# Kernel optimization log

Measured on AMD Instinct MI355X. Metric: run time of the kernel, lower is better.

## Reference

```python
import jax, jax.numpy as jnp
import numpy as np

# dims: n=batch, T=n_shifts, dX=16, dU=8, H=256 hidden, L=128 ldim, K=64 n_aux (L=2K)

def setup_inputs() -> dict:
    key = jax.random.key(0)
    ks = jax.random.split(key, 16)
    n, T, dX, dU, H, L, K = 64, 64, 16, 8, 256, 128, 64
    def lin(k, fan_in, shape):
        return (jax.random.uniform(k, shape, jnp.float32) * 2.0 - 1.0) / np.sqrt(fan_in)
    xs = jax.random.normal(ks[0], (n, T, dX), jnp.float32)
    us = jax.random.normal(ks[1], (n, T - 1, dU), jnp.float32)
    theta = jax.random.uniform(ks[2], (K,), jnp.float32) * (2.0 * np.pi)
    inp = {
        'xs': xs, 'us': us,
        # stacked x-aux encoders (K copies): BN affine, 3 linear layers (last no bias), output scale
        'x_gamma': jnp.ones((K, dX)), 'x_beta': jnp.zeros((K, dX)),
        'xW1': lin(ks[3], dX, (K, dX, H)), 'xb1': jnp.zeros((K, H)),
        'xW2': lin(ks[4], H, (K, H, H)), 'xb2': jnp.zeros((K, H)),
        'xW3': lin(ks[5], H, (K, H, L)), 'x_scale': jnp.ones((K, L)),
        # stacked u-aux encoders (K copies)
        'u_gamma': jnp.ones((K, dU)), 'u_beta': jnp.zeros((K, dU)),
        'uW1': lin(ks[6], dU, (K, dU, H)), 'ub1': jnp.zeros((K, H)),
        'uW2': lin(ks[7], H, (K, H, H)), 'ub2': jnp.zeros((K, H)),
        'uW3': lin(ks[8], H, (K, H, L)), 'u_scale': jnp.ones((K, L)),
        # Jordan-block complex eigenvalues (|lam| ~ 0.95)
        'reL': 0.95 * jnp.cos(theta), 'imL': 0.95 * jnp.sin(theta),
        # decoder C: Linear(ldim, dim, bias=False) -> weight [dX, L]
        'C_W': lin(ks[9], L, (dX, L)),
    }
    return inp


def _encoder(x, gamma, beta, W1, b1, W2, b2, W3, scale):
    # x: [M, D]; stacked params over K nets. BN stats (training mode) are per-feature over M,
    # identical across nets since the same x feeds every net.
    mu = x.mean(0)
    var = ((x - mu) ** 2).mean(0)
    xn = (x - mu) * jax.lax.rsqrt(var + 1e-5)          # [M, D]
    h = xn[None] * gamma[:, None, :] + beta[:, None, :]  # [K, M, D]
    h = jax.nn.leaky_relu(jnp.einsum('kmd,kdh->kmh', h, W1) + b1[:, None, :])
    h = jax.nn.leaky_relu(jnp.einsum('kmd,kdh->kmh', h, W2) + b2[:, None, :])
    h = jnp.einsum('kmd,kdh->kmh', h, W3)               # last layer: no bias
    return h * scale[:, None, :]                        # [K, M, L]


def reference(xs, us, x_gamma, x_beta, xW1, xb1, xW2, xb2, xW3, x_scale,
              u_gamma, u_beta, uW1, ub1, uW2, ub2, uW3, u_scale, reL, imL, C_W):
    n, T, dX = xs.shape
    K = reL.shape[0]
    L = 2 * K
    Tm1 = T - 1
    # phi1s: [n, T, K(net), K(pair), 2]
    phi = _encoder(xs.reshape(n * T, dX), x_gamma, x_beta, xW1, xb1, xW2, xb2, xW3, x_scale)
    phi1s = jnp.moveaxis(phi, 0, 1).reshape(n, T, K, K, 2)
    # ures = psi(u) - psi(0): [n, T-1, K, K, 2]
    uflat = us.reshape(n * Tm1, -1)
    psi_u = _encoder(uflat, u_gamma, u_beta, uW1, ub1, uW2, ub2, uW3, u_scale)
    psi_0 = _encoder(jnp.zeros_like(uflat), u_gamma, u_beta, uW1, ub1, uW2, ub2, uW3, u_scale)
    ures = jnp.moveaxis(psi_u - psi_0, 0, 1).reshape(n, Tm1, K, K, 2)
    # block-diagonal Koopman: per net j a 2x2 rotation-scale [[re, im], [-im, re]]
    R = jnp.stack([jnp.stack([reL, imL], -1), jnp.stack([-imL, reL], -1)], -2)  # [K, 2, 2]

    def step(p, u_t):
        p = jnp.einsum('bjkc,jcd->bjkd', p + u_t, R)
        return p, p

    _, preds = jax.lax.scan(step, phi1s[:, 0], jnp.moveaxis(ures, 0, 1))
    preds = jnp.moveaxis(preds, 0, 1)  # [n, T-1, K, K, 2]

    def phi2y(p):
        # sum over net axis (-3), flatten pair dims -> [.., L], decode with C
        return p.sum(-3).reshape(*p.shape[:-3], L) @ C_W.T

    y = phi2y(phi1s[:, 1:])
    y_pred = phi2y(preds)
    return y, y_pred
```

## Files before the change

kernel.cpp:

```cpp
#include <hip/hip_runtime.h>

typedef __bf16 bf16_t;
typedef __bf16 bf16x8 __attribute__((ext_vector_type(8)));
typedef __bf16 bf16x4 __attribute__((ext_vector_type(4)));
typedef float  f32x4  __attribute__((ext_vector_type(4)));

#define PHI_JS  (4096 * 128 + 64)
#define PSIU_JS (4032 * 128 + 64)

__global__ __launch_bounds__(256) void prep_all_kernel(
    const float* __restrict__ xW1, const float* __restrict__ xb1,
    const float* __restrict__ xg,  const float* __restrict__ xbeta,
    const float* __restrict__ uW1, const float* __restrict__ ub1,
    const float* __restrict__ ug,  const float* __restrict__ ubeta,
    const float* __restrict__ xW2, const float* __restrict__ uW2,
    const float* __restrict__ xW3, const float* __restrict__ uW3,
    const float* __restrict__ x_scale, const float* __restrict__ u_scale,
    const float* __restrict__ xs, const float* __restrict__ us,
    bf16_t* __restrict__ xW1t, float* __restrict__ xb1p,
    bf16_t* __restrict__ uW1t, float* __restrict__ ub1p,
    bf16_t* __restrict__ xW2t, bf16_t* __restrict__ uW2t,
    bf16_t* __restrict__ xW3t, bf16_t* __restrict__ uW3t,
    float* __restrict__ part, float* __restrict__ zout)
{
    const int t = blockIdx.x, tid = threadIdx.x;
    __shared__ float tile[32][33];
    __shared__ float h1[256], h2[256];

    if (t < 12288) {
        const float* in; bf16_t* outp; const float* scale = nullptr;
        int j, r0, c0, C;
        if (t < 8192) {
            C = 256;
            j = (t & 4095) >> 6;
            const int tl = t & 63; r0 = (tl >> 3) * 32; c0 = (tl & 7) * 32;
            if (t < 4096) { in = xW2; outp = xW2t; }
            else          { in = uW2; outp = uW2t; }
        } else {
            C = 128;
            const int l = t - 8192;
            j = (l & 2047) >> 5;
            const int tl = l & 31; r0 = (tl >> 2) * 32; c0 = (tl & 3) * 32;
            if (l < 2048) { in = xW3; outp = xW3t; scale = x_scale + j * 128; }
            else          { in = uW3; outp = uW3t; scale = u_scale + j * 128; }
        }
        const int R = 256;
        in   += (size_t)j * R * C;
        bf16_t* op = outp + (size_t)j * R * C;
        const int tx = tid & 31, ty = tid >> 5;
        #pragma unroll
        for (int i = 0; i < 4; i++)
            tile[ty + i * 8][tx] = in[(size_t)(r0 + ty + i * 8) * C + c0 + tx];
        __syncthreads();
        #pragma unroll
        for (int i = 0; i < 4; i++) {
            int c = c0 + ty + i * 8;
            float sc = scale ? scale[c] : 1.f;
            op[(size_t)c * R + r0 + tx] = (bf16_t)(tile[tx][ty + i * 8] * sc);
        }
    } else if (t < 12416) {
        const int bid = t - 12288, j = bid & 63, h = tid;
        const float *W1, *b1, *gamma, *beta; bf16_t* W1t; float* b1p; int D;
        if (bid < 64) { W1 = xW1; b1 = xb1; gamma = xg; beta = xbeta; W1t = xW1t; b1p = xb1p; D = 16; }
        else          { W1 = uW1; b1 = ub1; gamma = ug; beta = ubeta; W1t = uW1t; b1p = ub1p; D = 8; }
        float bacc = b1[j * 256 + h];
        bf16_t* orow = W1t + (size_t)(j * 256 + h) * 32;
        for (int d = 0; d < 32; d++) orow[d] = (bf16_t)0.f;
        for (int d = 0; d < D; d++) {
            float w = W1[((size_t)j * D + d) * 256 + h];
            orow[d] = (bf16_t)(gamma[j * D + d] * w);
            bacc += beta[j * D + d] * w;
        }
        b1p[j * 256 + h] = bacc;
    } else if (t < 12512) {
        const int bid = t - 12416;
        const bool isx = bid < 64;
        const float* x = isx ? xs : us;
        const int D   = isx ? 16 : 8;
        const int lb  = isx ? bid : bid - 64;
        const int per = isx ? 1024 : 1008;
        const int start = lb * per;
        float a = 0.f, b = 0.f;
        for (int idx = start + tid; idx < start + per; idx += 256) {
            float v = x[idx];
            a += v; b += v * v;
        }
        float* s1 = h1; float* s2 = h2;
        s1[tid] = a; s2[tid] = b;
        __syncthreads();
        if (tid < D) {
            float sa = 0.f, sb = 0.f;
            for (int k = tid; k < 256; k += D) { sa += s1[k]; sb += s2[k]; }
            part[bid * 32 + tid]      = sa;
            part[bid * 32 + 16 + tid] = sb;
        }
    } else {
        const int g = (t - 12512) * 256 + tid;
        for (int i = g; i < 2 * 64 * 63 * 16; i += 64 * 256)
            zout[i] = 0.f;
    }
}

__global__ __launch_bounds__(512, 4) void fused_mlp_kernel(
    const float* __restrict__ xs, const float* __restrict__ us,
    const float* __restrict__ part,
    const bf16_t* __restrict__ xW1t, const float* __restrict__ xb1p,
    const bf16_t* __restrict__ xW2t, const float* __restrict__ xb2,
    const bf16_t* __restrict__ xW3t,
    const bf16_t* __restrict__ uW1t, const float* __restrict__ ub1p,
    const bf16_t* __restrict__ uW2t, const float* __restrict__ ub2,
    const bf16_t* __restrict__ uW3t,
    const float* __restrict__ uW1r, const float* __restrict__ ub1r,
    const float* __restrict__ ubetar, const float* __restrict__ uW2r,
    const float* __restrict__ uW3r, const float* __restrict__ u_scaler,
    float* __restrict__ psi0_out,
    bf16_t* __restrict__ phi, bf16_t* __restrict__ psiu)
{
    const int bid  = blockIdx.x;
    const int tid  = threadIdx.x;

    __shared__ __align__(16) bf16_t hs[128 * 256];
    __shared__ float stats_s[32];

    if (bid >= 4096) {
        const int j = bid - 4096;
        float* fb  = (float*)hs;
        float* h1  = fb;
        float* h2  = fb + 256;
        float* tmp = fb + 512;
        const int h = tid & 255, half = tid >> 8;
        if (half == 0) {
            float bacc = ub1r[j * 256 + h];
            #pragma unroll
            for (int d = 0; d < 8; d++)
                bacc += ubetar[j * 8 + d] * uW1r[((size_t)j * 8 + d) * 256 + h];
            h1[h] = fmaxf(bacc, 0.01f * bacc);
        }
        __syncthreads();
        {
            float acc = (half == 0) ? ub2[j * 256 + h] : 0.f;
            const float* w2 = uW2r + (size_t)j * 65536 + (size_t)half * 128 * 256 + h;
            #pragma unroll 16
            for (int d = 0; d < 128; d++) acc += h1[half * 128 + d] * w2[(size_t)d * 256];
            tmp[tid] = acc;
        }
        __syncthreads();
        if (half == 0) {
            float v = tmp[h] + tmp[h + 256];
            h2[h] = fmaxf(v, 0.01f * v);
        }
        __syncthreads();
        {
            const int h3 = tid & 127, qd = tid >> 7;
            float acc = 0.f;
            const float* w3 = uW3r + (size_t)j * 32768 + (size_t)qd * 64 * 128 + h3;
            #pragma unroll 16
            for (int d = 0; d < 64; d++) acc += h2[qd * 64 + d] * w3[(size_t)d * 128];
            tmp[tid] = acc;
        }
        __syncthreads();
        if (tid < 128)
            psi0_out[j * 128 + tid] =
                (tmp[tid] + tmp[tid + 128] + tmp[tid + 256] + tmp[tid + 384])
                * u_scaler[j * 128 + tid];
        return;
    }

    const int xcd  = bid & 7;
    const int slot = bid >> 3;
    const int band = slot >> 6;
    const int t64  = slot & 63;
    const int j    = xcd * 8 + band;
    const bool is_x = t64 < 32;
    const int tile  = is_x ? t64 : (t64 - 32);

    const float*  In  = is_x ? xs   : us;
    const int     D   = is_x ? 16   : 8;
    const bf16_t* W1t = is_x ? xW1t : uW1t;
    const float*  b1p = is_x ? xb1p : ub1p;
    const bf16_t* W2t = is_x ? xW2t : uW2t;
    const float*  b2  = is_x ? xb2  : ub2;
    const bf16_t* W3t = is_x ? xW3t : uW3t;
    bf16_t* outp      = is_x ? phi  : psiu;
    const int M       = is_x ? 4096 : 4032;
    const size_t JS   = is_x ? (size_t)PHI_JS : (size_t)PSIU_JS;

    const int row0 = tile * 128;
    const int wave = tid >> 6;
    const int lane = tid & 63;
    const int quad = lane >> 4;
    const int l16  = lane & 15;
    const int lo2  = l16 & 3, hi2 = l16 >> 2;

    if (tid < 16) {
        if (is_x) {
            float sa = 0.f, sb = 0.f;
            #pragma unroll 8
            for (int b = 0; b < 64; b++) { sa += part[b * 32 + tid]; sb += part[b * 32 + 16 + tid]; }
            float mu = sa / 4096.f, var = sb / 4096.f - mu * mu;
            stats_s[tid] = mu; stats_s[16 + tid] = rsqrtf(var + 1e-5f);
        } else if (tid < 8) {
            float sa = 0.f, sb = 0.f;
            #pragma unroll 8
            for (int b = 64; b < 96; b++) { sa += part[b * 32 + tid]; sb += part[b * 32 + 16 + tid]; }
            float mu = sa / 4032.f, var = sb / 4032.f - mu * mu;
            stats_s[tid] = mu; stats_s[16 + tid] = rsqrtf(var + 1e-5f);
        }
    }
    __syncthreads();

    const f32x4 vzero = {0.f, 0.f, 0.f, 0.f};

    char* const hsB = (char*)hs;
    const char* const abase = hsB + l16 * 512 + ((quad ^ lo2) << 4);
    const int  wlow0 = (quad >> 1) ^ lo2;
    char* const wbase = hsB + l16 * 512 + ((wave ^ hi2) << 6) + ((quad & 1) << 3);

    {
        bf16x8 wfr[2];
        #pragma unroll
        for (int nbi = 0; nbi < 2; nbi++)
            wfr[nbi] = *reinterpret_cast<const bf16x8*>(
                W1t + (size_t)(j * 256 + wave * 32 + nbi * 16 + l16) * 32 + quad * 8);

        f32x4 acc[8][2];
        #pragma unroll
        for (int a = 0; a < 8; a++) { acc[a][0] = vzero; acc[a][1] = vzero; }

        const int c0 = quad * 8;
        #pragma unroll
        for (int mb = 0; mb < 8; mb++) {
            bf16x8 a;
            if (c0 < D) {
                int row = row0 + mb * 16 + l16;
                if (row > M - 1) row = M - 1;
                const float* xp = In + (size_t)row * D + c0;
                f32x4 v0 = *reinterpret_cast<const f32x4*>(xp);
                f32x4 v1 = *reinterpret_cast<const f32x4*>(xp + 4);
                #pragma unroll
                for (int e = 0; e < 4; e++) a[e]     = (bf16_t)((v0[e] - stats_s[c0 + e])     * stats_s[16 + c0 + e]);
                #pragma unroll
                for (int e = 0; e < 4; e++) a[4 + e] = (bf16_t)((v1[e] - stats_s[c0 + 4 + e]) * stats_s[16 + c0 + 4 + e]);
            } else {
                #pragma unroll
                for (int e = 0; e < 8; e++) a[e] = (bf16_t)0.f;
            }
            #pragma unroll
            for (int nbi = 0; nbi < 2; nbi++)
                acc[mb][nbi] = __builtin_amdgcn_mfma_f32_16x16x32_bf16(
                    wfr[nbi], a, acc[mb][nbi], 0, 0, 0);
        }

        #pragma unroll
        for (int nbi = 0; nbi < 2; nbi++) {
            const f32x4 bias = *reinterpret_cast<const f32x4*>(
                b1p + j * 256 + wave * 32 + nbi * 16 + quad * 4);
            char* wp = wbase + ((wlow0 ^ (nbi << 1)) << 4);
            #pragma unroll
            for (int mb = 0; mb < 8; mb++) {
                bf16x4 pk;
                #pragma unroll
                for (int r = 0; r < 4; r++) {
                    float v = acc[mb][nbi][r] + bias[r];
                    v = fmaxf(v, 0.01f * v);
                    pk[r] = (bf16_t)v;
                }
                *reinterpret_cast<bf16x4*>(wp + mb * 8192) = pk;
            }
        }
    }
    __syncthreads();

    {
        f32x4 acc[8][2];
        #pragma unroll
        for (int a = 0; a < 8; a++) { acc[a][0] = vzero; acc[a][1] = vzero; }

        const bf16_t* w2base = W2t + ((size_t)j * 256 + wave * 32 + l16) * 256 + quad * 8;

        bf16x8 wr[3][2];
        #pragma unroll
        for (int d = 0; d < 3; d++)
            #pragma unroll
            for (int nbi = 0; nbi < 2; nbi++)
                wr[d][nbi] = *reinterpret_cast<const bf16x8*>(w2base + nbi * 4096 + d * 32);

        #pragma unroll
        for (int kk = 0; kk < 8; kk++) {
            const int c = kk % 3;
            const char* ap = abase + ((kk ^ hi2) << 6);
            bf16x8 av0[4];
            #pragma unroll
            for (int mb = 0; mb < 4; mb++)
                av0[mb] = *reinterpret_cast<const bf16x8*>(ap + mb * 8192);
            #pragma unroll
            for (int nbi = 0; nbi < 2; nbi++)
                #pragma unroll
                for (int mb = 0; mb < 4; mb++)
                    acc[mb][nbi] = __builtin_amdgcn_mfma_f32_16x16x32_bf16(
                        wr[c][nbi], av0[mb], acc[mb][nbi], 0, 0, 0);
            bf16x8 av1[4];
            #pragma unroll
            for (int mb = 0; mb < 4; mb++)
                av1[mb] = *reinterpret_cast<const bf16x8*>(ap + (mb + 4) * 8192);
            #pragma unroll
            for (int nbi = 0; nbi < 2; nbi++)
                #pragma unroll
                for (int mb = 4; mb < 8; mb++)
                    acc[mb][nbi] = __builtin_amdgcn_mfma_f32_16x16x32_bf16(
                        wr[c][nbi], av1[mb - 4], acc[mb][nbi], 0, 0, 0);
            if (kk < 5) {
                #pragma unroll
                for (int nbi = 0; nbi < 2; nbi++)
                    wr[c][nbi] = *reinterpret_cast<const bf16x8*>(
                        w2base + nbi * 4096 + (kk + 3) * 32);
            }
        }
        __syncthreads();
        #pragma unroll
        for (int nbi = 0; nbi < 2; nbi++) {
            const f32x4 bias = *reinterpret_cast<const f32x4*>(
                b2 + j * 256 + wave * 32 + nbi * 16 + quad * 4);
            char* wp = wbase + ((wlow0 ^ (nbi << 1)) << 4);
            #pragma unroll
            for (int mb = 0; mb < 8; mb++) {
                bf16x4 pk;
                #pragma unroll
                for (int r = 0; r < 4; r++) {
                    float v = acc[mb][nbi][r] + bias[r];
                    v = fmaxf(v, 0.01f * v);
                    pk[r] = (bf16_t)v;
                }
                *reinterpret_cast<bf16x4*>(wp + mb * 8192) = pk;
            }
        }
    }
    __syncthreads();

    {
        f32x4 acc[8];
        #pragma unroll
        for (int a = 0; a < 8; a++) acc[a] = vzero;

        const bf16_t* w3base = W3t + ((size_t)j * 128 + wave * 16 + l16) * 256 + quad * 8;

        bf16x8 wr[3];
        #pragma unroll
        for (int d = 0; d < 3; d++)
            wr[d] = *reinterpret_cast<const bf16x8*>(w3base + d * 32);

        #pragma unroll
        for (int kk = 0; kk < 8; kk++) {
            const int c = kk % 3;
            const char* ap = abase + ((kk ^ hi2) << 6);
            bf16x8 av0[4];
            #pragma unroll
            for (int mb = 0; mb < 4; mb++)
                av0[mb] = *reinterpret_cast<const bf16x8*>(ap + mb * 8192);
            #pragma unroll
            for (int mb = 0; mb < 4; mb++)
                acc[mb] = __builtin_amdgcn_mfma_f32_16x16x32_bf16(
                    wr[c], av0[mb], acc[mb], 0, 0, 0);
            bf16x8 av1[4];
            #pragma unroll
            for (int mb = 0; mb < 4; mb++)
                av1[mb] = *reinterpret_cast<const bf16x8*>(ap + (mb + 4) * 8192);
            #pragma unroll
            for (int mb = 4; mb < 8; mb++)
                acc[mb] = __builtin_amdgcn_mfma_f32_16x16x32_bf16(
                    wr[c], av1[mb - 4], acc[mb], 0, 0, 0);
            if (kk < 5)
                wr[c] = *reinterpret_cast<const bf16x8*>(w3base + (kk + 3) * 32);
        }
        __syncthreads();
        {
            const int sp3 = (wave * 2 + (quad >> 1)) ^ l16;
            char* w3p = hsB + l16 * 256 + sp3 * 16 + ((quad & 1) << 3);
            #pragma unroll
            for (int mb = 0; mb < 8; mb++) {
                bf16x4 pk;
                #pragma unroll
                for (int r = 0; r < 4; r++) pk[r] = (bf16_t)acc[mb][r];
                *reinterpret_cast<bf16x4*>(w3p + mb * 4096) = pk;
            }
        }
    }
    __syncthreads();
    #pragma unroll
    for (int p = 0; p < 4; p++) {
        const int rr = p * 32 + (tid >> 4);
        const int s  = tid & 15;
        if (row0 + rr < M) {
            bf16x8 v = *reinterpret_cast<const bf16x8*>(hs + rr * 128 + (s ^ (rr & 15)) * 8);
            *reinterpret_cast<bf16x8*>(outp + (size_t)j * JS + (size_t)(row0 + rr) * 128 + s * 8) = v;
        }
    }
}

__global__ __launch_bounds__(256) void scan_kernel(
    const bf16_t* __restrict__ phi, const bf16_t* __restrict__ psiu,
    const float* __restrict__ psi0, const float* __restrict__ reL,
    const float* __restrict__ imL, const float* __restrict__ C_W,
    float* __restrict__ y, float* __restrict__ ypred) {
    const int b = blockIdx.x >> 3, jg = blockIdx.x & 7;
    const int tid = threadIdx.x;
    const int wave = tid >> 6, lane = tid & 63;
    __shared__ float redP[2][4][128];
    __shared__ float redY[2][4][128];
    __shared__ float SP[128], SY[128];
    __shared__ float Cs[2048];
    #pragma unroll
    for (int i = 0; i < 8; i++) Cs[tid + i * 256] = C_W[tid + i * 256];

    const int j0 = jg * 8 + wave * 2;
    float sx0, sy0, sx1, sy1;
    float p0x0, p0y0, p0x1, p0y1, lre0, lim0, lre1, lim1;
    {
        unsigned v0 = *reinterpret_cast<const unsigned*>(
            phi + (size_t)j0 * PHI_JS + (size_t)(b * 64) * 128 + lane * 2);
        unsigned v1 = *reinterpret_cast<const unsigned*>(
            phi + (size_t)(j0 + 1) * PHI_JS + (size_t)(b * 64) * 128 + lane * 2);
        sx0 = __uint_as_float(v0 << 16); sy0 = __uint_as_float(v0 & 0xFFFF0000u);
        sx1 = __uint_as_float(v1 << 16); sy1 = __uint_as_float(v1 & 0xFFFF0000u);
        float2 p0 = *reinterpret_cast<const float2*>(psi0 + j0 * 128 + lane * 2);
        float2 p1 = *reinterpret_cast<const float2*>(psi0 + (j0 + 1) * 128 + lane * 2);
        p0x0 = p0.x; p0y0 = p0.y; p0x1 = p1.x; p0y1 = p1.y;
        lre0 = reL[j0]; lim0 = imL[j0]; lre1 = reL[j0 + 1]; lim1 = imL[j0 + 1];
    }
    const bf16_t* up0 = psiu + (size_t)j0 * PSIU_JS + (size_t)(b * 63) * 128 + lane * 2;
    const bf16_t* up1 = psiu + (size_t)(j0 + 1) * PSIU_JS + (size_t)(b * 63) * 128 + lane * 2;
    const bf16_t* pp0 = phi + (size_t)j0 * PHI_JS + (size_t)(b * 64 + 1) * 128 + lane * 2;
    const bf16_t* pp1 = phi + (size_t)(j0 + 1) * PHI_JS + (size_t)(b * 64 + 1) * 128 + lane * 2;
    unsigned cur0 = *reinterpret_cast<const unsigned*>(up0);
    unsigned cur1 = *reinterpret_cast<const unsigned*>(up1);
    unsigned curp0 = *reinterpret_cast<const unsigned*>(pp0);
    unsigned curp1 = *reinterpret_cast<const unsigned*>(pp1);

    const int oo = (tid & 127) >> 3, qq = tid & 7;

    for (int t = 0; t < 63; t++) {
        unsigned nx0 = 0, nx1 = 0, np0 = 0, np1 = 0;
        if (t < 62) {
            nx0 = *reinterpret_cast<const unsigned*>(up0 + (t + 1) * 128);
            nx1 = *reinterpret_cast<const unsigned*>(up1 + (t + 1) * 128);
            np0 = *reinterpret_cast<const unsigned*>(pp0 + (t + 1) * 128);
            np1 = *reinterpret_cast<const unsigned*>(pp1 + (t + 1) * 128);
        }
        float px = sx0 + (__uint_as_float(cur0 << 16) - p0x0);
        float py = sy0 + (__uint_as_float(cur0 & 0xFFFF0000u) - p0y0);
        sx0 = px * lre0 - py * lim0;
        sy0 = px * lim0 + py * lre0;
        px = sx1 + (__uint_as_float(cur1 << 16) - p0x1);
        py = sy1 + (__uint_as_float(cur1 & 0xFFFF0000u) - p0y1);
        sx1 = px * lre1 - py * lim1;
        sy1 = px * lim1 + py * lre1;
        float yx = __uint_as_float(curp0 << 16) + __uint_as_float(curp1 << 16);
        float yy = __uint_as_float(curp0 & 0xFFFF0000u) + __uint_as_float(curp1 & 0xFFFF0000u);
        const int db = t & 1;
        redP[db][wave][lane * 2]     = sx0 + sx1;
        redP[db][wave][lane * 2 + 1] = sy0 + sy1;
        redY[db][wave][lane * 2]     = yx;
        redY[db][wave][lane * 2 + 1] = yy;
        __syncthreads();
        if (tid < 128)
            SP[tid] = redP[db][0][tid] + redP[db][1][tid]
                    + redP[db][2][tid] + redP[db][3][tid];
        else {
            const int tl = tid - 128;
            SY[tl] = redY[db][0][tl] + redY[db][1][tl]
                   + redY[db][2][tl] + redY[db][3][tl];
        }
        __syncthreads();
        {
            const float* S = (tid < 128) ? SP : SY;
            float acc = 0.f;
            #pragma unroll
            for (int i = 0; i < 16; i++)
                acc += S[qq * 16 + i] * Cs[oo * 128 + qq * 16 + i];
            acc += __shfl_xor(acc, 4, 8);
            acc += __shfl_xor(acc, 2, 8);
            acc += __shfl_xor(acc, 1, 8);
            if (qq == 0) {
                float* dst = (tid < 128) ? (ypred + (b * 63 + t) * 16 + oo)
                                         : (y     + (b * 63 + t) * 16 + oo);
                atomicAdd(dst, acc);
            }
        }
        cur0 = nx0; cur1 = nx1; curp0 = np0; curp1 = np1;
    }
}

extern "C" void kernel_launch(void* const* d_in, const int* in_sizes, int n_in,
                              void* d_out, int out_size, void* d_ws, size_t ws_size,
                              hipStream_t stream) {
    const float* xs      = (const float*)d_in[0];
    const float* us      = (const float*)d_in[1];
    const float* x_gamma = (const float*)d_in[2];
    const float* x_beta  = (const float*)d_in[3];
    const float* xW1     = (const float*)d_in[4];
    const float* xb1     = (const float*)d_in[5];
    const float* xW2     = (const float*)d_in[6];
    const float* xb2     = (const float*)d_in[7];
    const float* xW3     = (const float*)d_in[8];
    const float* x_scale = (const float*)d_in[9];
    const float* u_gamma = (const float*)d_in[10];
    const float* u_beta  = (const float*)d_in[11];
    const float* uW1     = (const float*)d_in[12];
    const float* ub1     = (const float*)d_in[13];
    const float* uW2     = (const float*)d_in[14];
    const float* ub2     = (const float*)d_in[15];
    const float* uW3     = (const float*)d_in[16];
    const float* u_scale = (const float*)d_in[17];
    const float* reL     = (const float*)d_in[18];
    const float* imL     = (const float*)d_in[19];
    const float* C_W     = (const float*)d_in[20];

    char* ws = (char*)d_ws;
    size_t off = 0;
    auto alloc = [&](size_t bytes) -> char* {
        char* p = ws + off;
        off += (bytes + 255) & ~(size_t)255;
        return p;
    };
    float*  part = (float*)alloc(96 * 32 * 4);
    bf16_t* xW1t = (bf16_t*)alloc((size_t)64 * 256 * 32 * 2);
    float*  xb1p = (float*) alloc((size_t)64 * 256 * 4);
    bf16_t* xW2t = (bf16_t*)alloc((size_t)64 * 256 * 256 * 2);
    bf16_t* xW3t = (bf16_t*)alloc((size_t)64 * 128 * 256 * 2);
    bf16_t* uW1t = (bf16_t*)alloc((size_t)64 * 256 * 32 * 2);
    float*  ub1p = (float*) alloc((size_t)64 * 256 * 4);
    bf16_t* uW2t = (bf16_t*)alloc((size_t)64 * 256 * 256 * 2);
    bf16_t* uW3t = (bf16_t*)alloc((size_t)64 * 128 * 256 * 2);
    float*  psi0 = (float*) alloc((size_t)64 * 128 * 4);
    bf16_t* phi  = (bf16_t*)alloc((size_t)64 * PHI_JS  * 2);
    bf16_t* psiu = (bf16_t*)alloc((size_t)64 * PSIU_JS * 2);

    float* y_out     = (float*)d_out;
    float* ypred_out = y_out + 64 * 63 * 16;

    prep_all_kernel<<<12576, 256, 0, stream>>>(
        xW1, xb1, x_gamma, x_beta, uW1, ub1, u_gamma, u_beta,
        xW2, uW2, xW3, uW3, x_scale, u_scale, xs, us,
        xW1t, xb1p, uW1t, ub1p, xW2t, uW2t, xW3t, uW3t, part, y_out);
    fused_mlp_kernel<<<4160, 512, 0, stream>>>(
        xs, us, part,
        xW1t, xb1p, xW2t, xb2, xW3t, uW1t, ub1p, uW2t, ub2, uW3t,
        uW1, ub1, u_beta, uW2, uW3, u_scale, psi0,
        phi, psiu);
    scan_kernel<<<512, 256, 0, stream>>>(
        phi, psiu, psi0, reL, imL, C_W, y_out, ypred_out);
}
```

Baseline: 357.2 us.

## Widen scan kernel to one net per wave and batch decoder over 8 steps

The scan kernel now runs 512 threads with one latent net per wave instead of two, and prefetches inputs two timesteps ahead. The C-decoding matvec is deferred and batched across 8 timesteps using a transposed C in shared memory, which removes one barrier per step and the per-step shuffle reductions. In exchange the reduction sums 8 partials and larger shared buffers are needed, and the batched decode runs a serial 128-term dot product per thread.

```diff
diff --git a/kernel.cpp b/kernel.cpp
--- a/kernel.cpp
+++ b/kernel.cpp
@@ -397,7 +397,7 @@
     }
 }
 
-__global__ __launch_bounds__(256) void scan_kernel(
+__global__ __launch_bounds__(512) void scan_kernel(
     const bf16_t* __restrict__ phi, const bf16_t* __restrict__ psiu,
     const float* __restrict__ psi0, const float* __restrict__ reL,
     const float* __restrict__ imL, const float* __restrict__ C_W,
@@ -405,88 +405,83 @@
     const int b = blockIdx.x >> 3, jg = blockIdx.x & 7;
     const int tid = threadIdx.x;
     const int wave = tid >> 6, lane = tid & 63;
-    __shared__ float redP[2][4][128];
-    __shared__ float redY[2][4][128];
-    __shared__ float SP[128], SY[128];
-    __shared__ float Cs[2048];
+    __shared__ float redP[2][8][128];
+    __shared__ float redY[2][8][128];
+    __shared__ float SPb[8][132];
+    __shared__ float SYb[8][132];
+    __shared__ float CsT[2048];
     #pragma unroll
-    for (int i = 0; i < 8; i++) Cs[tid + i * 256] = C_W[tid + i * 256];
-
-    const int j0 = jg * 8 + wave * 2;
-    float sx0, sy0, sx1, sy1;
-    float p0x0, p0y0, p0x1, p0y1, lre0, lim0, lre1, lim1;
+    for (int i = 0; i < 4; i++) {
+        const int idx = tid + i * 512;
+        CsT[(idx & 127) * 16 + (idx >> 7)] = C_W[idx];
+    }
+
+    const int j0 = jg * 8 + wave;
+    float sx, sy, p0x, p0y, lre, lim;
     {
-        unsigned v0 = *reinterpret_cast<const unsigned*>(
+        unsigned v = *reinterpret_cast<const unsigned*>(
             phi + (size_t)j0 * PHI_JS + (size_t)(b * 64) * 128 + lane * 2);
-        unsigned v1 = *reinterpret_cast<const unsigned*>(
-            phi + (size_t)(j0 + 1) * PHI_JS + (size_t)(b * 64) * 128 + lane * 2);
-        sx0 = __uint_as_float(v0 << 16); sy0 = __uint_as_float(v0 & 0xFFFF0000u);
-        sx1 = __uint_as_float(v1 << 16); sy1 = __uint_as_float(v1 & 0xFFFF0000u);
+        sx = __uint_as_float(v << 16); sy = __uint_as_float(v & 0xFFFF0000u);
         float2 p0 = *reinterpret_cast<const float2*>(psi0 + j0 * 128 + lane * 2);
-        float2 p1 = *reinterpret_cast<const float2*>(psi0 + (j0 + 1) * 128 + lane * 2);
-        p0x0 = p0.x; p0y0 = p0.y; p0x1 = p1.x; p0y1 = p1.y;
-        lre0 = reL[j0]; lim0 = imL[j0]; lre1 = reL[j0 + 1]; lim1 = imL[j0 + 1];
-    }
-    const bf16_t* up0 = psiu + (size_t)j0 * PSIU_JS + (size_t)(b * 63) * 128 + lane * 2;
-    const bf16_t* up1 = psiu + (size_t)(j0 + 1) * PSIU_JS + (size_t)(b * 63) * 128 + lane * 2;
-    const bf16_t* pp0 = phi + (size_t)j0 * PHI_JS + (size_t)(b * 64 + 1) * 128 + lane * 2;
-    const bf16_t* pp1 = phi + (size_t)(j0 + 1) * PHI_JS + (size_t)(b * 64 + 1) * 128 + lane * 2;
-    unsigned cur0 = *reinterpret_cast<const unsigned*>(up0);
-    unsigned cur1 = *reinterpret_cast<const unsigned*>(up1);
-    unsigned curp0 = *reinterpret_cast<const unsigned*>(pp0);
-    unsigned curp1 = *reinterpret_cast<const unsigned*>(pp1);
-
-    const int oo = (tid & 127) >> 3, qq = tid & 7;
-
+        p0x = p0.x; p0y = p0.y;
+        lre = reL[j0]; lim = imL[j0];
+    }
+    const bf16_t* up = psiu + (size_t)j0 * PSIU_JS + (size_t)(b * 63) * 128 + lane * 2;
+    const bf16_t* pp = phi  + (size_t)j0 * PHI_JS  + (size_t)(b * 64 + 1) * 128 + lane * 2;
+    unsigned cu0 = *reinterpret_cast<const unsigned*>(up);
+    unsigned cp0 = *reinterpret_cast<const unsigned*>(pp);
+    unsigned nu1 = *reinterpret_cast<const unsigned*>(up + 128);
+    unsigned np1 = *reinterpret_cast<const unsigned*>(pp + 128);
+
+    const int ds  = (tid >> 7) & 1;
+    const int dr  = tid & 127;
+    const int dtt = dr >> 4, doo = dr & 15;
+
+    int tbase = 0;
     for (int t = 0; t < 63; t++) {
-        unsigned nx0 = 0, nx1 = 0, np0 = 0, np1 = 0;
-        if (t < 62) {
-            nx0 = *reinterpret_cast<const unsigned*>(up0 + (t + 1) * 128);
-            nx1 = *reinterpret_cast<const unsigned*>(up1 + (t + 1) * 128);
-            np0 = *reinterpret_cast<const unsigned*>(pp0 + (t + 1) * 128);
-            np1 = *reinterpret_cast<const unsigned*>(pp1 + (t + 1) * 128);
-        }
-        float px = sx0 + (__uint_as_float(cur0 << 16) - p0x0);
-        float py = sy0 + (__uint_as_float(cur0 & 0xFFFF0000u) - p0y0);
-        sx0 = px * lre0 - py * lim0;
-        sy0 = px * lim0 + py * lre0;
-        px = sx1 + (__uint_as_float(cur1 << 16) - p0x1);
-        py = sy1 + (__uint_as_float(cur1 & 0xFFFF0000u) - p0y1);
-        sx1 = px * lre1 - py * lim1;
-        sy1 = px * lim1 + py * lre1;
-        float yx = __uint_as_float(curp0 << 16) + __uint_as_float(curp1 << 16);
-        float yy = __uint_as_float(curp0 & 0xFFFF0000u) + __uint_as_float(curp1 & 0xFFFF0000u);
+        unsigned nu2 = 0, np2 = 0;
+        if (t < 61) {
+            nu2 = *reinterpret_cast<const unsigned*>(up + (t + 2) * 128);
+            np2 = *reinterpret_cast<const unsigned*>(pp + (t + 2) * 128);
+        }
+        float px = sx + (__uint_as_float(cu0 << 16) - p0x);
+        float py = sy + (__uint_as_float(cu0 & 0xFFFF0000u) - p0y);
+        sx = px * lre - py * lim;
+        sy = px * lim + py * lre;
+        const float yx = __uint_as_float(cp0 << 16);
+        const float yy = __uint_as_float(cp0 & 0xFFFF0000u);
         const int db = t & 1;
-        redP[db][wave][lane * 2]     = sx0 + sx1;
-        redP[db][wave][lane * 2 + 1] = sy0 + sy1;
+        redP[db][wave][lane * 2]     = sx;
+        redP[db][wave][lane * 2 + 1] = sy;
         redY[db][wave][lane * 2]     = yx;
         redY[db][wave][lane * 2 + 1] = yy;
         __syncthreads();
-        if (tid < 128)
-            SP[tid] = redP[db][0][tid] + redP[db][1][tid]
-                    + redP[db][2][tid] + redP[db][3][tid];
-        else {
+        const int slot = t & 7;
+        if (tid < 128) {
+            SPb[slot][tid] =
+                redP[db][0][tid] + redP[db][1][tid] + redP[db][2][tid] + redP[db][3][tid]
+              + redP[db][4][tid] + redP[db][5][tid] + redP[db][6][tid] + redP[db][7][tid];
+        } else if (tid < 256) {
             const int tl = tid - 128;
-            SY[tl] = redY[db][0][tl] + redY[db][1][tl]
-                   + redY[db][2][tl] + redY[db][3][tl];
-        }
-        __syncthreads();
-        {
-            const float* S = (tid < 128) ? SP : SY;
-            float acc = 0.f;
-            #pragma unroll
-            for (int i = 0; i < 16; i++)
-                acc += S[qq * 16 + i] * Cs[oo * 128 + qq * 16 + i];
-            acc += __shfl_xor(acc, 4, 8);
-            acc += __shfl_xor(acc, 2, 8);
-            acc += __shfl_xor(acc, 1, 8);
-            if (qq == 0) {
-                float* dst = (tid < 128) ? (ypred + (b * 63 + t) * 16 + oo)
-                                         : (y     + (b * 63 + t) * 16 + oo);
+            SYb[slot][tl] =
+                redY[db][0][tl] + redY[db][1][tl] + redY[db][2][tl] + redY[db][3][tl]
+              + redY[db][4][tl] + redY[db][5][tl] + redY[db][6][tl] + redY[db][7][tl];
+        }
+        cu0 = nu1; cp0 = np1; nu1 = nu2; np1 = np2;
+        if (slot == 7 || t == 62) {
+            __syncthreads();
+            if (tid < 256 && dtt <= slot) {
+                const float* S = ds ? SYb[dtt] : SPb[dtt];
+                float acc = 0.f;
+                #pragma unroll
+                for (int i = 0; i < 128; i++) acc += S[i] * CsT[i * 16 + doo];
+                float* dst = ds ? (y     + (b * 63 + tbase + dtt) * 16 + doo)
+                                : (ypred + (b * 63 + tbase + dtt) * 16 + doo);
                 atomicAdd(dst, acc);
             }
-        }
-        cur0 = nx0; cur1 = nx1; curp0 = np0; curp1 = np1;
+            __syncthreads();
+            tbase = t + 1;
+        }
     }
 }
 
@@ -547,6 +542,6 @@
         xW1t, xb1p, xW2t, xb2, xW3t, uW1t, ub1p, uW2t, ub2, uW3t,
         uW1, ub1, u_beta, uW2, uW3, u_scale, psi0,
         phi, psiu);
-    scan_kernel<<<512, 256, 0, stream>>>(
+    scan_kernel<<<512, 512, 0, stream>>>(
         phi, psiu, psi0, reL, imL, C_W, y_out, ypred_out);
 }
```

Result: faster. 343.9 us (-3.7%).
